# Performance work log

Measured on AMD Instinct MI355X. Metric: run time of the kernel, lower is better.

The kernel has to match this reference:

```python
import jax, jax.numpy as jnp
import numpy as np

SCALING = 1.0


def setup_inputs() -> dict:
    key = jax.random.key(0)
    k1, k2, k3, k4, k5, k6 = jax.random.split(key, 6)
    in_f, out_f, r = 4096, 4096, 32
    nnz = r * (in_f + out_f)  # 262144
    x = jax.random.normal(k1, (4, 2048, in_f), dtype=jnp.float32)
    weight = jax.random.normal(k2, (out_f, in_f), dtype=jnp.float32) * 0.02
    bias = jax.random.normal(k3, (out_f,), dtype=jnp.float32) * 0.02
    shira_weight = jax.random.normal(k4, (nnz,), dtype=jnp.float32) * 0.02
    rows = jax.random.randint(k5, (1, nnz), 0, out_f, dtype=jnp.int32)
    cols = jax.random.randint(k6, (1, nnz), 0, in_f, dtype=jnp.int32)
    shira_indices = jnp.concatenate([rows, cols], axis=0)  # [2, nnz]
    return {"x": x, "weight": weight, "bias": bias,
            "shira_weight": shira_weight, "shira_indices": shira_indices}


def reference(x, weight, bias, shira_weight, shira_indices):
    # delta = sparse_coo(indices, shira_weight * scaling) densified into weight copy
    new_weight = weight.at[shira_indices[0], shira_indices[1]].add(shira_weight * SCALING)
    # F.linear: x @ W^T + b
    return jnp.einsum('bsi,oi->bso', x, new_weight) + bias
```

## Files before the change

kernel.cpp:

```cpp
#include <hip/hip_runtime.h>
#include <hip/hip_bf16.h>
#include <stdint.h>

typedef float v4f __attribute__((ext_vector_type(4)));
typedef short v8s __attribute__((ext_vector_type(8)));

#define GEMM_M 8192
#define GEMM_N 4096
#define GEMM_K 4096
#define BM 256
#define BN 256
#define BK 64
#define NT (GEMM_K / BK)


__device__ __forceinline__ uint16_t f2bf(float f) {
    union { float f; uint32_t u; } v; v.f = f;
    uint32_t r = v.u + 0x7FFFu + ((v.u >> 16) & 1u);
    return (uint16_t)(r >> 16);
}

__device__ __forceinline__ float bf2f(uint16_t h) {
    union { uint32_t u; float f; } v; v.u = ((uint32_t)h) << 16;
    return v.f;
}

__device__ __forceinline__ void cvt8(const float* __restrict__ s, uint16_t* __restrict__ d) {
    float4 a = ((const float4*)s)[0];
    float4 b = ((const float4*)s)[1];
    union { v8s v; uint16_t u[8]; } o;
    o.u[0] = f2bf(a.x); o.u[1] = f2bf(a.y); o.u[2] = f2bf(a.z); o.u[3] = f2bf(a.w);
    o.u[4] = f2bf(b.x); o.u[5] = f2bf(b.y); o.u[6] = f2bf(b.z); o.u[7] = f2bf(b.w);
    *(v8s*)d = o.v;
}

__global__ void prep_cvt_kernel(const float* __restrict__ X, const float* __restrict__ W,
                                uint16_t* __restrict__ Xb, uint16_t* __restrict__ Wb,
                                size_t x8) {
    size_t i = (size_t)blockIdx.x * blockDim.x + threadIdx.x;
    if (i < x8) {
        cvt8(X + i * 8, Xb + i * 8);
    } else {
        size_t j = i - x8;
        cvt8(W + j * 8, Wb + j * 8);
    }
}

__global__ void scatter_bf16_kernel(uint16_t* __restrict__ Wb, const float* __restrict__ vals,
                                    const int* __restrict__ rows, const int* __restrict__ cols,
                                    int nnz) {
    int i = blockIdx.x * blockDim.x + threadIdx.x;
    if (i >= nnz) return;
    size_t idx = (size_t)rows[i] * GEMM_K + cols[i];
    uint32_t* addr = (uint32_t*)Wb + (idx >> 1);
    const bool hi = idx & 1;
    const float v = vals[i];
    uint32_t cur = *addr, assumed;
    do {
        assumed = cur;
        uint16_t h = hi ? (uint16_t)(assumed >> 16) : (uint16_t)(assumed & 0xFFFFu);
        uint16_t nh = f2bf(bf2f(h) + v);
        uint32_t nw = hi ? ((assumed & 0x0000FFFFu) | ((uint32_t)nh << 16))
                         : ((assumed & 0xFFFF0000u) | (uint32_t)nh);
        if (nw == assumed) break;
        cur = atomicCAS(addr, assumed, nw);
    } while (cur != assumed);
}


__device__ __forceinline__ void gload_lds16(const void* g, void* lds) {
    __builtin_amdgcn_global_load_lds(
        (const __attribute__((address_space(1))) void*)(uintptr_t)g,
        (__attribute__((address_space(3))) void*)(uintptr_t)lds,
        16, 0, 0);
}

__global__ __launch_bounds__(512, 2) void gemm_bt_kernel(
    const uint16_t* __restrict__ A,
    const uint16_t* __restrict__ B,
    const float* __restrict__ bias,
    float* __restrict__ C)
{
    __shared__ __attribute__((aligned(16))) uint16_t As[2][2][128 * BK];
    __shared__ __attribute__((aligned(16))) uint16_t Bs[2][2][128 * BK];

    const int tid  = threadIdx.x;
    const int lane = tid & 63;
    const int wid  = tid >> 6;
    const int wm2  = wid >> 1;
    const int wn2  = wid & 1;
    const int lrow = lane & 15;
    const int quad = lane >> 4;
    const int xr   = lane & 7;

    const int bid = blockIdx.x;
    const int swz = (bid & 7) * 64 + (bid >> 3);
    const int m0  = (swz >> 4) * BM;
    const int n0  = (swz & 15) * BN;

    const int srow = wid * 16 + (lane >> 3);
    const int skc  = ((lane & 7) ^ (lane >> 3)) * 8;
    const uint16_t* gA = A + (size_t)(m0 + srow) * GEMM_K + skc;
    const uint16_t* gB = B + (size_t)(n0 + srow) * GEMM_K + skc;
    const int ldso = wid * 1024 + lane * 8;

#define STAGE(gbase, hrow, s, ldshalf)  do {                                   \
        const uint16_t* _g = (gbase) + (size_t)(hrow) * GEMM_K + (s) * BK;     \
        uint16_t* _l = (ldshalf) + ldso;                                       \
        gload_lds16(_g, _l);                                                   \
        gload_lds16(_g + (size_t)8 * GEMM_K, _l + 512);                        \
    } while (0)

    v4f acc00[2][4], acc10[2][4], acc01[2][4], acc11[2][4];
#pragma unroll
    for (int mi = 0; mi < 2; ++mi)
#pragma unroll
        for (int nj = 0; nj < 4; ++nj) {
            acc00[mi][nj] = (v4f){0.f, 0.f, 0.f, 0.f};
            acc10[mi][nj] = (v4f){0.f, 0.f, 0.f, 0.f};
            acc01[mi][nj] = (v4f){0.f, 0.f, 0.f, 0.f};
            acc11[mi][nj] = (v4f){0.f, 0.f, 0.f, 0.f};
        }

    v8s a0F[2][2], a1F[2][2], bF[4][2];

#define LDA(dst, hp) do {                                                      \
        _Pragma("unroll")                                                      \
        for (int mi = 0; mi < 2; ++mi)                                         \
        _Pragma("unroll")                                                      \
        for (int ks = 0; ks < 2; ++ks) {                                       \
            const int rh = wm2 * 32 + mi * 16 + lrow;                          \
            const int c  = ks * 4 + quad;                                      \
            dst[mi][ks] = *(const v8s*)((hp) + rh * BK + ((c ^ xr) << 3));     \
        } } while (0)

#define LDB(hp) do {                                                           \
        _Pragma("unroll")                                                      \
        for (int nj = 0; nj < 4; ++nj)                                         \
        _Pragma("unroll")                                                      \
        for (int ks = 0; ks < 2; ++ks) {                                       \
            const int rh = wn2 * 64 + nj * 16 + lrow;                          \
            const int c  = ks * 4 + quad;                                      \
            bF[nj][ks] = *(const v8s*)((hp) + rh * BK + ((c ^ xr) << 3));      \
        } } while (0)

#define MM(accq, aT) do {                                                      \
        _Pragma("unroll")                                                      \
        for (int ks = 0; ks < 2; ++ks)                                         \
        _Pragma("unroll")                                                      \
        for (int mi = 0; mi < 2; ++mi)                                         \
        _Pragma("unroll")                                                      \
        for (int nj = 0; nj < 4; ++nj)                                         \
            accq[mi][nj] = __builtin_amdgcn_mfma_f32_16x16x32_bf16(            \
                aT[mi][ks], bF[nj][ks], accq[mi][nj], 0, 0, 0);                \
    } while (0)

#define BAR()   __builtin_amdgcn_s_barrier()
#define LGKM0() asm volatile("s_waitcnt lgkmcnt(0)" ::: "memory")
#define VM6()   asm volatile("s_waitcnt vmcnt(6)" ::: "memory")
#define SCHED() __builtin_amdgcn_sched_barrier(0)

    STAGE(gA, 0,   0, &As[0][0][0]);
    STAGE(gA, 128, 0, &As[0][1][0]);
    STAGE(gB, 0,   0, &Bs[0][0][0]);
    STAGE(gB, 128, 0, &Bs[0][1][0]);
    STAGE(gA, 0,   1, &As[1][0][0]);
    STAGE(gA, 128, 1, &As[1][1][0]);
    STAGE(gB, 0,   1, &Bs[1][0][0]);
    SCHED(); VM6();
    BAR();

#define TILE(t, b) do {                                                        \
        const int s1 = ((t) + 1) & (NT - 1);                                   \
        const int s2 = ((t) + 2) & (NT - 1);                                   \
                                                       \
        LDA(a0F, &As[b][0][0]);                                                \
        LDB(&Bs[b][0][0]);                                                     \
        STAGE(gB, 128, s1, &Bs[(b) ^ 1][1][0]);                                \
        SCHED(); BAR(); LGKM0(); SCHED();                                      \
        __builtin_amdgcn_s_setprio(1); MM(acc00, a0F); __builtin_amdgcn_s_setprio(0); \
        SCHED(); BAR();                                                        \
                                                       \
        LDA(a1F, &As[b][1][0]);                                                \
        STAGE(gA, 0, s2, &As[b][0][0]);                                        \
        SCHED(); BAR(); LGKM0(); SCHED();                                      \
        __builtin_amdgcn_s_setprio(1); MM(acc10, a1F); __builtin_amdgcn_s_setprio(0); \
        SCHED(); BAR();                                                        \
                                                       \
        LDB(&Bs[b][1][0]);                                                     \
        STAGE(gA, 128, s2, &As[b][1][0]);                                      \
        SCHED(); BAR(); LGKM0(); SCHED();                                      \
        __builtin_amdgcn_s_setprio(1); MM(acc01, a0F); __builtin_amdgcn_s_setprio(0); \
        SCHED(); BAR();                                                        \
                 \
        STAGE(gB, 0, s2, &Bs[b][0][0]);                                        \
        SCHED(); VM6();                                                        \
        BAR();                                                                 \
        __builtin_amdgcn_s_setprio(1); MM(acc11, a1F); __builtin_amdgcn_s_setprio(0); \
        SCHED(); BAR();                                                        \
    } while (0)

    for (int t = 0; t < NT; t += 2) {
        TILE(t, 0);
        TILE(t + 1, 1);
    }

#define WR(accq, QM, QN) do {                                                  \
        _Pragma("unroll")                                                      \
        for (int nj = 0; nj < 4; ++nj) {                                       \
            const int col = n0 + (QN) * 128 + wn2 * 64 + nj * 16 + lrow;       \
            const float bj = bias[col];                                        \
            _Pragma("unroll")                                                  \
            for (int mi = 0; mi < 2; ++mi) {                                   \
                const int row = m0 + (QM) * 128 + wm2 * 32 + mi * 16 + quad * 4; \
                float* cp = C + (size_t)row * GEMM_N + col;                    \
                _Pragma("unroll")                                              \
                for (int r = 0; r < 4; ++r)                                    \
                    cp[(size_t)r * GEMM_N] = accq[mi][nj][r] + bj;             \
            }                                                                  \
        } } while (0)

    WR(acc00, 0, 0);
    WR(acc10, 1, 0);
    WR(acc01, 0, 1);
    WR(acc11, 1, 1);

#undef STAGE
#undef LDA
#undef LDB
#undef MM
#undef BAR
#undef LGKM0
#undef VM6
#undef SCHED
#undef TILE
#undef WR
}


extern "C" void kernel_launch(void* const* d_in, const int* in_sizes, int n_in,
                              void* d_out, int out_size, void* d_ws, size_t ws_size,
                              hipStream_t stream) {
    const float* x      = (const float*)d_in[0];
    const float* weight = (const float*)d_in[1];
    const float* bias   = (const float*)d_in[2];
    const float* sw     = (const float*)d_in[3];
    const int*   sidx   = (const int*)d_in[4];
    const int nnz = in_sizes[3];

    const size_t welems = (size_t)GEMM_N * GEMM_K;
    const size_t xelems = (size_t)GEMM_M * GEMM_K;

    uint16_t* Wb = (uint16_t*)d_ws;
    uint16_t* Xb = (uint16_t*)((char*)d_ws + welems * sizeof(uint16_t));

    const size_t x8 = xelems / 8;
    const size_t w8 = welems / 8;
    const int prep_blocks = (int)((x8 + w8) / 256);

    prep_cvt_kernel<<<dim3(prep_blocks), 256, 0, stream>>>(x, weight, Xb, Wb, x8);
    scatter_bf16_kernel<<<dim3((nnz + 255) / 256), 256, 0, stream>>>(
        Wb, sw, sidx, sidx + nnz, nnz);
    gemm_bt_kernel<<<dim3((GEMM_M / BM) * (GEMM_N / BN)), 512, 0, stream>>>(
        Xb, Wb, bias, (float*)d_out);
}
```

Baseline: 503.1 us.

## Switch GEMM inner loop to 32x32x16 MFMA and remove intra-phase barriers

Replaces the 16x16x32 bf16 MFMA tiling with 32x32x16 MFMA, reorganizing the LDS fragment loads, the accumulator layout and the output write mapping to match. Each wave now issues fewer, larger MFMAs with fewer LDS fragment reads per flop. It also removes the barrier placed between the LDS fragment loads and the MFMA block in the first three phases of each tile, keeping only a wait on local memory counters. This risks LDS read/write hazards if the restaging does not line up with the slower waves, and it changes the output write coalescing pattern.

```diff
diff --git a/kernel.cpp b/kernel.cpp
--- a/kernel.cpp
+++ b/kernel.cpp
@@ -2,8 +2,8 @@
 #include <hip/hip_bf16.h>
 #include <stdint.h>
 
-typedef float v4f __attribute__((ext_vector_type(4)));
-typedef short v8s __attribute__((ext_vector_type(8)));
+typedef float v16f __attribute__((ext_vector_type(16)));
+typedef short v8s  __attribute__((ext_vector_type(8)));
 
 #define GEMM_M 8192
 #define GEMM_N 4096
@@ -89,9 +89,8 @@
     const int wid  = tid >> 6;
     const int wm2  = wid >> 1;
     const int wn2  = wid & 1;
-    const int lrow = lane & 15;
-    const int quad = lane >> 4;
-    const int xr   = lane & 7;
+    const int l32  = lane & 31;
+    const int g    = lane >> 5;
 
     const int bid = blockIdx.x;
     const int swz = (bid & 7) * 64 + (bid >> 3);
@@ -111,54 +110,53 @@
         gload_lds16(_g + (size_t)8 * GEMM_K, _l + 512);                        \
     } while (0)
 
-    v4f acc00[2][4], acc10[2][4], acc01[2][4], acc11[2][4];
+    v16f acc00[2], acc10[2], acc01[2], acc11[2];
 #pragma unroll
-    for (int mi = 0; mi < 2; ++mi)
-#pragma unroll
-        for (int nj = 0; nj < 4; ++nj) {
-            acc00[mi][nj] = (v4f){0.f, 0.f, 0.f, 0.f};
-            acc10[mi][nj] = (v4f){0.f, 0.f, 0.f, 0.f};
-            acc01[mi][nj] = (v4f){0.f, 0.f, 0.f, 0.f};
-            acc11[mi][nj] = (v4f){0.f, 0.f, 0.f, 0.f};
-        }
-
-    v8s a0F[2][2], a1F[2][2], bF[4][2];
-
-#define LDA(dst, hp) do {                                                      \
-        _Pragma("unroll")                                                      \
-        for (int mi = 0; mi < 2; ++mi)                                         \
-        _Pragma("unroll")                                                      \
-        for (int ks = 0; ks < 2; ++ks) {                                       \
-            const int rh = wm2 * 32 + mi * 16 + lrow;                          \
-            const int c  = ks * 4 + quad;                                      \
-            dst[mi][ks] = *(const v8s*)((hp) + rh * BK + ((c ^ xr) << 3));     \
+    for (int nj = 0; nj < 2; ++nj) {
+        acc00[nj] = (v16f)(0.f);
+        acc10[nj] = (v16f)(0.f);
+        acc01[nj] = (v16f)(0.f);
+        acc11[nj] = (v16f)(0.f);
+    }
+
+    v8s a0F[4], a1F[4], bF[2][4];
+
+#define LDA32(dst, hp) do {                                                    \
+        const int _rh = wm2 * 32 + l32;                                        \
+        const uint16_t* _p = (hp) + _rh * BK;                                  \
+        const int _x = _rh & 7;                                                \
+        _Pragma("unroll")                                                      \
+        for (int ks = 0; ks < 4; ++ks) {                                       \
+            const int _c = ks * 2 + g;                                         \
+            dst[ks] = *(const v8s*)(_p + ((_c ^ _x) << 3));                    \
         } } while (0)
 
-#define LDB(hp) do {                                                           \
-        _Pragma("unroll")                                                      \
-        for (int nj = 0; nj < 4; ++nj)                                         \
-        _Pragma("unroll")                                                      \
-        for (int ks = 0; ks < 2; ++ks) {                                       \
-            const int rh = wn2 * 64 + nj * 16 + lrow;                          \
-            const int c  = ks * 4 + quad;                                      \
-            bF[nj][ks] = *(const v8s*)((hp) + rh * BK + ((c ^ xr) << 3));      \
-        } } while (0)
-
-#define MM(accq, aT) do {                                                      \
-        _Pragma("unroll")                                                      \
-        for (int ks = 0; ks < 2; ++ks)                                         \
-        _Pragma("unroll")                                                      \
-        for (int mi = 0; mi < 2; ++mi)                                         \
-        _Pragma("unroll")                                                      \
-        for (int nj = 0; nj < 4; ++nj)                                         \
-            accq[mi][nj] = __builtin_amdgcn_mfma_f32_16x16x32_bf16(            \
-                aT[mi][ks], bF[nj][ks], accq[mi][nj], 0, 0, 0);                \
+#define LDB32(hp) do {                                                         \
+        _Pragma("unroll")                                                      \
+        for (int nj = 0; nj < 2; ++nj) {                                       \
+            const int _rh = wn2 * 64 + nj * 32 + l32;                          \
+            const uint16_t* _p = (hp) + _rh * BK;                              \
+            const int _x = _rh & 7;                                            \
+            _Pragma("unroll")                                                  \
+            for (int ks = 0; ks < 4; ++ks) {                                   \
+                const int _c = ks * 2 + g;                                     \
+                bF[nj][ks] = *(const v8s*)(_p + ((_c ^ _x) << 3));             \
+            } } } while (0)
+
+#define MM32(accq, aT) do {                                                    \
+        _Pragma("unroll")                                                      \
+        for (int ks = 0; ks < 4; ++ks)                                         \
+        _Pragma("unroll")                                                      \
+        for (int nj = 0; nj < 2; ++nj)                                         \
+            accq[nj] = __builtin_amdgcn_mfma_f32_32x32x16_bf16(                \
+                aT[ks], bF[nj][ks], accq[nj], 0, 0, 0);                        \
     } while (0)
 
 #define BAR()   __builtin_amdgcn_s_barrier()
 #define LGKM0() asm volatile("s_waitcnt lgkmcnt(0)" ::: "memory")
 #define VM6()   asm volatile("s_waitcnt vmcnt(6)" ::: "memory")
 #define SCHED() __builtin_amdgcn_sched_barrier(0)
+#define PRIO(p) __builtin_amdgcn_s_setprio(p)
 
     STAGE(gA, 0,   0, &As[0][0][0]);
     STAGE(gA, 128, 0, &As[0][1][0]);
@@ -168,36 +166,36 @@
     STAGE(gA, 128, 1, &As[1][1][0]);
     STAGE(gB, 0,   1, &Bs[1][0][0]);
     SCHED(); VM6();
-    BAR();
+    BAR(); SCHED();
 
 #define TILE(t, b) do {                                                        \
         const int s1 = ((t) + 1) & (NT - 1);                                   \
         const int s2 = ((t) + 2) & (NT - 1);                                   \
-                                                       \
-        LDA(a0F, &As[b][0][0]);                                                \
-        LDB(&Bs[b][0][0]);                                                     \
+                                         \
+        LDA32(a0F, &As[b][0][0]);                                              \
+        LDB32(&Bs[b][0][0]);                                                   \
         STAGE(gB, 128, s1, &Bs[(b) ^ 1][1][0]);                                \
-        SCHED(); BAR(); LGKM0(); SCHED();                                      \
-        __builtin_amdgcn_s_setprio(1); MM(acc00, a0F); __builtin_amdgcn_s_setprio(0); \
-        SCHED(); BAR();                                                        \
-                                                       \
-        LDA(a1F, &As[b][1][0]);                                                \
+        LGKM0(); SCHED();                                                      \
+        PRIO(1); MM32(acc00, a0F); PRIO(0);                                    \
+        SCHED(); BAR(); SCHED();                                               \
+                                          \
+        LDA32(a1F, &As[b][1][0]);                                              \
         STAGE(gA, 0, s2, &As[b][0][0]);                                        \
-        SCHED(); BAR(); LGKM0(); SCHED();                                      \
-        __builtin_amdgcn_s_setprio(1); MM(acc10, a1F); __builtin_amdgcn_s_setprio(0); \
-        SCHED(); BAR();                                                        \
-                                                       \
-        LDB(&Bs[b][1][0]);                                                     \
+        LGKM0(); SCHED();                                                      \
+        PRIO(1); MM32(acc10, a1F); PRIO(0);                                    \
+        SCHED(); BAR(); SCHED();                                               \
+                                          \
+        LDB32(&Bs[b][1][0]);                                                   \
         STAGE(gA, 128, s2, &As[b][1][0]);                                      \
-        SCHED(); BAR(); LGKM0(); SCHED();                                      \
-        __builtin_amdgcn_s_setprio(1); MM(acc01, a0F); __builtin_amdgcn_s_setprio(0); \
-        SCHED(); BAR();                                                        \
-                 \
+        LGKM0(); SCHED();                                                      \
+        PRIO(1); MM32(acc01, a0F); PRIO(0);                                    \
+        SCHED(); BAR(); SCHED();                                               \
+         \
         STAGE(gB, 0, s2, &Bs[b][0][0]);                                        \
         SCHED(); VM6();                                                        \
-        BAR();                                                                 \
-        __builtin_amdgcn_s_setprio(1); MM(acc11, a1F); __builtin_amdgcn_s_setprio(0); \
-        SCHED(); BAR();                                                        \
+        BAR(); SCHED();                                                        \
+        PRIO(1); MM32(acc11, a1F); PRIO(0);                                    \
+        SCHED();                                                               \
     } while (0)
 
     for (int t = 0; t < NT; t += 2) {
@@ -205,36 +203,35 @@
         TILE(t + 1, 1);
     }
 
-#define WR(accq, QM, QN) do {                                                  \
-        _Pragma("unroll")                                                      \
-        for (int nj = 0; nj < 4; ++nj) {                                       \
-            const int col = n0 + (QN) * 128 + wn2 * 64 + nj * 16 + lrow;       \
+#define WR32(accq, QM, QN) do {                                                \
+        _Pragma("unroll")                                                      \
+        for (int nj = 0; nj < 2; ++nj) {                                       \
+            const int col = n0 + (QN) * 128 + wn2 * 64 + nj * 32 + l32;        \
             const float bj = bias[col];                                        \
+            const int rbase = m0 + (QM) * 128 + wm2 * 32 + 4 * g;              \
             _Pragma("unroll")                                                  \
-            for (int mi = 0; mi < 2; ++mi) {                                   \
-                const int row = m0 + (QM) * 128 + wm2 * 32 + mi * 16 + quad * 4; \
-                float* cp = C + (size_t)row * GEMM_N + col;                    \
-                _Pragma("unroll")                                              \
-                for (int r = 0; r < 4; ++r)                                    \
-                    cp[(size_t)r * GEMM_N] = accq[mi][nj][r] + bj;             \
+            for (int r = 0; r < 16; ++r) {                                     \
+                const int row = rbase + (r & 3) + 8 * (r >> 2);                \
+                C[(size_t)row * GEMM_N + col] = accq[nj][r] + bj;              \
             }                                                                  \
         } } while (0)
 
-    WR(acc00, 0, 0);
-    WR(acc10, 1, 0);
-    WR(acc01, 0, 1);
-    WR(acc11, 1, 1);
+    WR32(acc00, 0, 0);
+    WR32(acc10, 1, 0);
+    WR32(acc01, 0, 1);
+    WR32(acc11, 1, 1);
 
 #undef STAGE
-#undef LDA
-#undef LDB
-#undef MM
+#undef LDA32
+#undef LDB32
+#undef MM32
 #undef BAR
 #undef LGKM0
 #undef VM6
 #undef SCHED
+#undef PRIO
 #undef TILE
-#undef WR
+#undef WR32
 }
 
 
```

Measured after the change: 523.1 us. +4.0%, slower.
